# Performance work log

Hardware: AMD Instinct MI355X
Metric: run time of the kernel (lower is better)

The kernel has to match this reference:

```python
import jax, jax.numpy as jnp
import numpy as np

ROWS, COLS, H, W = 128, 128, 128, 128
B, C = 2, 16
DENSITY = 0.01  # classic Hough vote matrix is very sparse binary


def setup_inputs() -> dict:
    key = jax.random.key(0)
    k_img, k_vote = jax.random.split(key)
    image = jax.random.normal(k_img, (B, C, ROWS, COLS), dtype=jnp.float32)
    # sparse binary voting matrix, shape (rows, cols, h, w)
    vote_index = (jax.random.uniform(k_vote, (ROWS, COLS, H, W)) < DENSITY).astype(jnp.float32)
    return {"image": image, "vote_index": vote_index}


def reference(image, vote_index):
    rows, cols, h, w = vote_index.shape
    b, c = image.shape[0], image.shape[1]
    V = vote_index.reshape(rows * cols, h * w)          # (rows*cols, h*w)
    x = jax.nn.relu(image.reshape(b * c, rows * cols))  # (b*c, rows*cols)
    ht = (x @ V) / cols                                 # (b*c, h*w)
    return ht.reshape(b, c, h, w)
```

## Files before the change

### kernel.cpp

```cpp
#include <hip/hip_runtime.h>

constexpr int Mdim = 32;
constexpr int Kdim = 16384;
constexpr int Ndim = 16384;

constexpr int TPB  = 256;
constexpr int NPT  = 2;
constexpr int NT   = TPB * NPT;
constexpr int NTILES = Ndim / NT;
constexpr int U    = 8;

__global__ __launch_bounds__(TPB)
void build_xt(const float* __restrict__ image, float* __restrict__ xT) {
    const int t = blockIdx.x * TPB + threadIdx.x;
    const int k = t >> 5;
    const int m = t & 31;
    const float v = image[(size_t)m * Kdim + k];
    xT[t] = fmaxf(v, 0.0f) * (1.0f / 128.0f);
}

__global__ __launch_bounds__(TPB, 4)
void ht_gemm(const float* __restrict__ xT,
             const float* __restrict__ vote,
             float* __restrict__ parts,
             int KC)
{
    const int tid    = threadIdx.x;
    const int ntile  = blockIdx.x % NTILES;
    const int kchunk = blockIdx.x / NTILES;
    const int k0     = kchunk * KC;
    const int n0     = ntile * NT + tid * NPT;

    const float* __restrict__ xk = xT + (size_t)k0 * Mdim;
    const float* __restrict__ vp = vote + (size_t)k0 * Ndim + n0;

    float2 acc[Mdim];
    #pragma unroll
    for (int m = 0; m < Mdim; ++m) acc[m] = make_float2(0.f, 0.f);

    float2 vbuf[U];
    #pragma unroll
    for (int u = 0; u < U; ++u)
        vbuf[u] = *reinterpret_cast<const float2*>(vp + (size_t)u * Ndim);

    for (int kk = 0; kk < KC - U; kk += U) {
        #pragma unroll
        for (int u = 0; u < U; ++u) {
            const float2 v = vbuf[u];
            vbuf[u] = *reinterpret_cast<const float2*>(vp + (size_t)(kk + U + u) * Ndim);
            const float* __restrict__ xrow = xk + (kk + u) * Mdim;
            #pragma unroll
            for (int m = 0; m < Mdim; ++m) {
                const float s = xrow[m];
                acc[m].x = fmaf(s, v.x, acc[m].x);
                acc[m].y = fmaf(s, v.y, acc[m].y);
            }
        }
    }
    {
        const int kk = KC - U;
        #pragma unroll
        for (int u = 0; u < U; ++u) {
            const float2 v = vbuf[u];
            const float* __restrict__ xrow = xk + (kk + u) * Mdim;
            #pragma unroll
            for (int m = 0; m < Mdim; ++m) {
                const float s = xrow[m];
                acc[m].x = fmaf(s, v.x, acc[m].x);
                acc[m].y = fmaf(s, v.y, acc[m].y);
            }
        }
    }

    float* p = parts + ((size_t)kchunk * Mdim) * Ndim + n0;
    #pragma unroll
    for (int m = 0; m < Mdim; ++m)
        *reinterpret_cast<float2*>(p + (size_t)m * Ndim) = acc[m];
}

__global__ __launch_bounds__(TPB)
void ht_reduce(const float* __restrict__ parts, float* __restrict__ out, int KT) {
    const size_t i4 = (size_t)blockIdx.x * TPB + threadIdx.x;
    const float4* p = reinterpret_cast<const float4*>(parts) + i4;
    float4 s = make_float4(0.f, 0.f, 0.f, 0.f);
    constexpr size_t stride4 = (size_t)Mdim * Ndim / 4;
    for (int c = 0; c < KT; ++c) {
        const float4 v = p[(size_t)c * stride4];
        s.x += v.x; s.y += v.y; s.z += v.z; s.w += v.w;
    }
    reinterpret_cast<float4*>(out)[i4] = s;
}

__global__ __launch_bounds__(TPB)
void ht_gemm_atomic(const float* __restrict__ image, const float* __restrict__ vote,
                    float* __restrict__ out) {
    __shared__ float xs[256 * Mdim];
    const int tid = threadIdx.x;
    const int ntile = blockIdx.x % 16;
    const int k0 = (blockIdx.x / 16) * 256;
    const int n0 = ntile * 1024 + tid * 4;
    for (int idx = tid; idx < 256 * Mdim; idx += TPB) {
        const int kk = idx >> 5, m = idx & 31;
        xs[idx] = fmaxf(image[(size_t)m * Kdim + (k0 + kk)], 0.0f) * (1.0f / 128.0f);
    }
    __syncthreads();
    float4 acc[Mdim];
    #pragma unroll
    for (int m = 0; m < Mdim; ++m) acc[m] = make_float4(0.f, 0.f, 0.f, 0.f);
    const float* vptr = vote + (size_t)k0 * Ndim + n0;
    for (int kk = 0; kk < 256; ++kk) {
        const float4 v = *reinterpret_cast<const float4*>(vptr);
        vptr += Ndim;
        #pragma unroll
        for (int m = 0; m < Mdim; ++m) {
            const float s = xs[kk * Mdim + m];
            acc[m].x = fmaf(s, v.x, acc[m].x); acc[m].y = fmaf(s, v.y, acc[m].y);
            acc[m].z = fmaf(s, v.z, acc[m].z); acc[m].w = fmaf(s, v.w, acc[m].w);
        }
    }
    #pragma unroll
    for (int m = 0; m < Mdim; ++m) {
        float* o = out + (size_t)m * Ndim + n0;
        unsafeAtomicAdd(o + 0, acc[m].x); unsafeAtomicAdd(o + 1, acc[m].y);
        unsafeAtomicAdd(o + 2, acc[m].z); unsafeAtomicAdd(o + 3, acc[m].w);
    }
}

extern "C" void kernel_launch(void* const* d_in, const int* in_sizes, int n_in,
                              void* d_out, int out_size, void* d_ws, size_t ws_size,
                              hipStream_t stream) {
    const float* image = (const float*)d_in[0];
    const float* vote  = (const float*)d_in[1];
    float* out = (float*)d_out;

    const size_t xt_bytes    = (size_t)Kdim * Mdim * sizeof(float);
    const size_t chunk_bytes = (size_t)Mdim * Ndim * sizeof(float);

    int KT = 0;
    for (int cand : {32, 16, 8, 4, 2}) {
        if (xt_bytes + (size_t)cand * chunk_bytes <= ws_size) { KT = cand; break; }
    }

    if (KT == 0) {
        (void)hipMemsetAsync(out, 0, (size_t)out_size * sizeof(float), stream);
        ht_gemm_atomic<<<dim3(16 * 64), TPB, 0, stream>>>(image, vote, out);
        return;
    }

    float* xT    = (float*)d_ws;
    float* parts = (float*)((char*)d_ws + xt_bytes);
    const int KC = Kdim / KT;

    build_xt<<<dim3((Kdim * Mdim) / TPB), TPB, 0, stream>>>(image, xT);
    ht_gemm<<<dim3(NTILES * KT), TPB, 0, stream>>>(xT, vote, parts, KC);
    ht_reduce<<<dim3((Mdim * Ndim) / (4 * TPB)), TPB, 0, stream>>>(parts, out, KT);
}
```

Measured before the change: 1.423 ms.

## Stage x tiles in double-buffered shared memory with float4 reads in split-K GEMM

```diff
diff --git a/kernel.cpp b/kernel.cpp
--- a/kernel.cpp
+++ b/kernel.cpp
@@ -8,7 +8,11 @@
 constexpr int NPT  = 2;
 constexpr int NT   = TPB * NPT;
 constexpr int NTILES = Ndim / NT;
-constexpr int U    = 8;
+constexpr int KT   = 32;
+constexpr int KC   = Kdim / KT;
+constexpr int SKC  = 128;
+constexpr int NSUB = KC / SKC;
+constexpr int U    = 4;
 
 __global__ __launch_bounds__(TPB)
 void build_xt(const float* __restrict__ image, float* __restrict__ xT) {
@@ -22,52 +26,66 @@
 __global__ __launch_bounds__(TPB, 4)
 void ht_gemm(const float* __restrict__ xT,
              const float* __restrict__ vote,
-             float* __restrict__ parts,
-             int KC)
+             float* __restrict__ parts)
 {
+    __shared__ float xs[2][SKC * Mdim];
+
     const int tid    = threadIdx.x;
     const int ntile  = blockIdx.x % NTILES;
     const int kchunk = blockIdx.x / NTILES;
     const int k0     = kchunk * KC;
     const int n0     = ntile * NT + tid * NPT;
 
-    const float* __restrict__ xk = xT + (size_t)k0 * Mdim;
-    const float* __restrict__ vp = vote + (size_t)k0 * Ndim + n0;
+    {
+        const float4* src = reinterpret_cast<const float4*>(xT + (size_t)k0 * Mdim);
+        float4* dst = reinterpret_cast<float4*>(xs[0]);
+        #pragma unroll
+        for (int i = 0; i < 4; ++i) dst[tid + TPB * i] = src[tid + TPB * i];
+    }
 
     float2 acc[Mdim];
     #pragma unroll
     for (int m = 0; m < Mdim; ++m) acc[m] = make_float2(0.f, 0.f);
 
+    const float* vp0 = vote + (size_t)k0 * Ndim + n0;
     float2 vbuf[U];
     #pragma unroll
     for (int u = 0; u < U; ++u)
-        vbuf[u] = *reinterpret_cast<const float2*>(vp + (size_t)u * Ndim);
+        vbuf[u] = *reinterpret_cast<const float2*>(vp0 + (size_t)u * Ndim);
+    const float* vpf = vp0 + (size_t)U * Ndim;
+    int kpf = k0 + U;
 
-    for (int kk = 0; kk < KC - U; kk += U) {
-        #pragma unroll
-        for (int u = 0; u < U; ++u) {
-            const float2 v = vbuf[u];
-            vbuf[u] = *reinterpret_cast<const float2*>(vp + (size_t)(kk + U + u) * Ndim);
-            const float* __restrict__ xrow = xk + (kk + u) * Mdim;
+    for (int c = 0; c < NSUB; ++c) {
+        __syncthreads();
+        if (c + 1 < NSUB) {
+            const float4* src = reinterpret_cast<const float4*>(
+                xT + (size_t)(k0 + (c + 1) * SKC) * Mdim);
+            float4* dst = reinterpret_cast<float4*>(xs[(c + 1) & 1]);
             #pragma unroll
-            for (int m = 0; m < Mdim; ++m) {
-                const float s = xrow[m];
-                acc[m].x = fmaf(s, v.x, acc[m].x);
-                acc[m].y = fmaf(s, v.y, acc[m].y);
-            }
+            for (int i = 0; i < 4; ++i) dst[tid + TPB * i] = src[tid + TPB * i];
         }
-    }
-    {
-        const int kk = KC - U;
-        #pragma unroll
-        for (int u = 0; u < U; ++u) {
-            const float2 v = vbuf[u];
-            const float* __restrict__ xrow = xk + (kk + u) * Mdim;
+
+        const float* xbase = xs[c & 1];
+        #pragma unroll 4
+        for (int kk = 0; kk < SKC; ++kk) {
+            const float2 v = vbuf[kk & (U - 1)];
+            vbuf[kk & (U - 1)] = *reinterpret_cast<const float2*>(vpf);
+            const bool adv = (kpf < Kdim - 1);
+            vpf += adv ? (size_t)Ndim : 0;
+            kpf += adv ? 1 : 0;
+
+            const float4* xrow = reinterpret_cast<const float4*>(xbase + kk * Mdim);
             #pragma unroll
-            for (int m = 0; m < Mdim; ++m) {
-                const float s = xrow[m];
-                acc[m].x = fmaf(s, v.x, acc[m].x);
-                acc[m].y = fmaf(s, v.y, acc[m].y);
+            for (int g = 0; g < 8; ++g) {
+                const float4 xv = xrow[g];
+                acc[4 * g + 0].x = fmaf(xv.x, v.x, acc[4 * g + 0].x);
+                acc[4 * g + 0].y = fmaf(xv.x, v.y, acc[4 * g + 0].y);
+                acc[4 * g + 1].x = fmaf(xv.y, v.x, acc[4 * g + 1].x);
+                acc[4 * g + 1].y = fmaf(xv.y, v.y, acc[4 * g + 1].y);
+                acc[4 * g + 2].x = fmaf(xv.z, v.x, acc[4 * g + 2].x);
+                acc[4 * g + 2].y = fmaf(xv.z, v.y, acc[4 * g + 2].y);
+                acc[4 * g + 3].x = fmaf(xv.w, v.x, acc[4 * g + 3].x);
+                acc[4 * g + 3].y = fmaf(xv.w, v.y, acc[4 * g + 3].y);
             }
         }
     }
@@ -79,12 +97,12 @@
 }
 
 __global__ __launch_bounds__(TPB)
-void ht_reduce(const float* __restrict__ parts, float* __restrict__ out, int KT) {
+void ht_reduce(const float* __restrict__ parts, float* __restrict__ out, int nchunks) {
     const size_t i4 = (size_t)blockIdx.x * TPB + threadIdx.x;
     const float4* p = reinterpret_cast<const float4*>(parts) + i4;
     float4 s = make_float4(0.f, 0.f, 0.f, 0.f);
     constexpr size_t stride4 = (size_t)Mdim * Ndim / 4;
-    for (int c = 0; c < KT; ++c) {
+    for (int c = 0; c < nchunks; ++c) {
         const float4 v = p[(size_t)c * stride4];
         s.x += v.x; s.y += v.y; s.z += v.z; s.w += v.w;
     }
@@ -94,14 +112,14 @@
 __global__ __launch_bounds__(TPB)
 void ht_gemm_atomic(const float* __restrict__ image, const float* __restrict__ vote,
                     float* __restrict__ out) {
-    __shared__ float xs[256 * Mdim];
+    __shared__ float xsh[256 * Mdim];
     const int tid = threadIdx.x;
     const int ntile = blockIdx.x % 16;
     const int k0 = (blockIdx.x / 16) * 256;
     const int n0 = ntile * 1024 + tid * 4;
     for (int idx = tid; idx < 256 * Mdim; idx += TPB) {
         const int kk = idx >> 5, m = idx & 31;
-        xs[idx] = fmaxf(image[(size_t)m * Kdim + (k0 + kk)], 0.0f) * (1.0f / 128.0f);
+        xsh[idx] = fmaxf(image[(size_t)m * Kdim + (k0 + kk)], 0.0f) * (1.0f / 128.0f);
     }
     __syncthreads();
     float4 acc[Mdim];
@@ -113,7 +131,7 @@
         vptr += Ndim;
         #pragma unroll
         for (int m = 0; m < Mdim; ++m) {
-            const float s = xs[kk * Mdim + m];
+            const float s = xsh[kk * Mdim + m];
             acc[m].x = fmaf(s, v.x, acc[m].x); acc[m].y = fmaf(s, v.y, acc[m].y);
             acc[m].z = fmaf(s, v.z, acc[m].z); acc[m].w = fmaf(s, v.w, acc[m].w);
         }
@@ -136,12 +154,7 @@
     const size_t xt_bytes    = (size_t)Kdim * Mdim * sizeof(float);
     const size_t chunk_bytes = (size_t)Mdim * Ndim * sizeof(float);
 
-    int KT = 0;
-    for (int cand : {32, 16, 8, 4, 2}) {
-        if (xt_bytes + (size_t)cand * chunk_bytes <= ws_size) { KT = cand; break; }
-    }
-
-    if (KT == 0) {
+    if (xt_bytes + (size_t)KT * chunk_bytes > ws_size) {
         (void)hipMemsetAsync(out, 0, (size_t)out_size * sizeof(float), stream);
         ht_gemm_atomic<<<dim3(16 * 64), TPB, 0, stream>>>(image, vote, out);
         return;
@@ -149,9 +162,8 @@
 
     float* xT    = (float*)d_ws;
     float* parts = (float*)((char*)d_ws + xt_bytes);
-    const int KC = Kdim / KT;
 
     build_xt<<<dim3((Kdim * Mdim) / TPB), TPB, 0, stream>>>(image, xT);
-    ht_gemm<<<dim3(NTILES * KT), TPB, 0, stream>>>(xT, vote, parts, KC);
+    ht_gemm<<<dim3(NTILES * KT), TPB, 0, stream>>>(xT, vote, parts);
     ht_reduce<<<dim3((Mdim * Ndim) / (4 * TPB)), TPB, 0, stream>>>(parts, out, KT);
 }
```

Result: slower. 2.003 ms (+40.7%).
